# Kernel tuning notes

Hardware: AMD Instinct MI355X
Metric: run time of the kernel (lower is better)

## Reference

```python
import jax, jax.numpy as jnp
import numpy as np

T, D, F, FS, E = 2048, 1024, 2048, 2048, 8
TOP_K = 1


def setup_inputs() -> dict:
    key = jax.random.key(0)
    ks = jax.random.split(key, 8)
    sd = 1.0 / np.sqrt(D)
    sf = 1.0 / np.sqrt(F)
    sfs = 1.0 / np.sqrt(FS)
    return {
        "hidden_states": jax.random.normal(ks[0], (T, D), jnp.float32),
        "router_w": jax.random.normal(ks[1], (E, D), jnp.float32) * sd,     # Linear(D->E), no bias
        "w_gate": jax.random.normal(ks[2], (E, D, F), jnp.float32) * sd,    # fused gate half
        "w_up": jax.random.normal(ks[3], (E, D, F), jnp.float32) * sd,      # fused up half
        "w_down": jax.random.normal(ks[4], (E, F, D), jnp.float32) * sf,
        "ws_gate": jax.random.normal(ks[5], (D, FS), jnp.float32) * sd,
        "ws_up": jax.random.normal(ks[6], (D, FS), jnp.float32) * sd,
        "ws_down": jax.random.normal(ks[7], (FS, D), jnp.float32) * sfs,
    }


def reference(hidden_states, router_w, w_gate, w_up, w_down, ws_gate, ws_up, ws_down):
    # Router: logits -> top-k -> sigmoid of top-k values (Llama4RenormalizeMoeRoutingMethod)
    logits = hidden_states @ router_w.T                      # [T, E]
    top_vals, top_idx = jax.lax.top_k(logits, TOP_K)         # [T, K]
    scores = jax.nn.sigmoid(top_vals.astype(jnp.float32)).astype(hidden_states.dtype)
    # Combine weights [T, E]; apply_router_weight_on_input=True -> scale INPUT per routed copy
    combine = (jax.nn.one_hot(top_idx, E, dtype=hidden_states.dtype) * scores[..., None]).sum(axis=1)
    xe = combine.T[:, :, None] * hidden_states[None]          # [E, T, D] (zero for non-routed tokens)
    g = jnp.einsum('etd,edf->etf', xe, w_gate)
    u = jnp.einsum('etd,edf->etf', xe, w_up)
    routed = jnp.einsum('etf,efd->etd', jax.nn.silu(g) * u, w_down).sum(axis=0)  # [T, D]
    # Shared expert (GatedMLP, SiLU)
    shared = (jax.nn.silu(hidden_states @ ws_gate) * (hidden_states @ ws_up)) @ ws_down
    return shared + routed
```

## Files before the change

### kernel.cpp

```cpp
#include <hip/hip_runtime.h>
#include <hip/hip_bf16.h>
#include <cstdint>
#include <cstddef>

#define T_TOK 2048
#define DIM   1024
#define FDIM  2048
#define NEXP  8

#define GU_MAX 48
#define DN_MAX 64

typedef short  short8  __attribute__((ext_vector_type(8)));
typedef float  floatx4 __attribute__((ext_vector_type(4)));

__device__ inline unsigned short f2bf(float f) {
    unsigned int u = __builtin_bit_cast(unsigned int, f);
    unsigned int r = (u + 0x7FFFu + ((u >> 16) & 1u)) >> 16;
    return (unsigned short)r;
}

__device__ inline unsigned int cvtpk(float a, float b) {
    unsigned int r;
    asm("v_cvt_pk_bf16_f32 %0, %1, %2" : "=v"(r) : "v"(a), "v"(b));
    return r;
}

__device__ inline void glds16(const void* g, const unsigned short* lds_base, int elem_off) {
    int u = __builtin_amdgcn_readfirstlane(elem_off);
    __builtin_amdgcn_global_load_lds(
        (const __attribute__((address_space(1))) unsigned int*)g,
        (__attribute__((address_space(3))) unsigned int*)(lds_base + u), 16, 0, 0);
}

__global__ __launch_bounds__(256) void k_router(
    const float* __restrict__ h, const float* __restrict__ rw,
    int* __restrict__ counts, int* __restrict__ lists,
    unsigned short* __restrict__ hb, unsigned short* __restrict__ xb)
{
    int w = threadIdx.x >> 6, lane = threadIdx.x & 63;
    int t = blockIdx.x * 4 + w;
    const float* hrow = h + (size_t)t * DIM;
    float hv[16];
    #pragma unroll
    for (int i = 0; i < 16; ++i) hv[i] = hrow[lane + 64 * i];
    float acc[NEXP];
    #pragma unroll
    for (int e = 0; e < NEXP; ++e) {
        const float* r = rw + (size_t)e * DIM;
        float s = 0.f;
        #pragma unroll
        for (int i = 0; i < 16; ++i) s += hv[i] * r[lane + 64 * i];
        acc[e] = s;
    }
    #pragma unroll
    for (int e = 0; e < NEXP; ++e) {
        float s = acc[e];
        for (int off = 32; off > 0; off >>= 1) s += __shfl_down(s, off);
        acc[e] = s;
    }
    float score = 0.f;
    if (lane == 0) {
        int be = 0; float bv = acc[0];
        #pragma unroll
        for (int e = 1; e < NEXP; ++e) if (acc[e] > bv) { bv = acc[e]; be = e; }
        score = 1.f / (1.f + __expf(-bv));
        int pos = atomicAdd(&counts[be], 1);
        lists[be * T_TOK + pos] = t;
    }
    score = __shfl(score, 0);
    unsigned short* hbr = hb + (size_t)t * DIM;
    unsigned short* xbr = xb + (size_t)t * DIM;
    #pragma unroll
    for (int i = 0; i < 16; ++i) {
        hbr[lane + 64 * i] = f2bf(hv[i]);
        xbr[lane + 64 * i] = f2bf(score * hv[i]);
    }
}

__global__ void k_schedule(const int* __restrict__ counts,
                           int* __restrict__ gu, int* __restrict__ dn)
{
    if (threadIdx.x != 0 || blockIdx.x != 0) return;
    int n = 0;
    for (int e = 0; e < NEXP; ++e) {
        int c = counts[e];
        for (int r = 0; r < c; r += 128) gu[n++] = (e << 16) | r;
    }
    for (int r = 0; r < T_TOK; r += 128) gu[n++] = (NEXP << 16) | r;
    while (n < GU_MAX) gu[n++] = -1;
    n = 0;
    for (int e = 0; e < NEXP; ++e) {
        int c = counts[e];
        for (int r = 0; r < c; r += 128) {
            dn[n++] = (e << 16) | r;
            dn[n++] = (1 << 28) | (e << 16) | r;
        }
    }
    while (n < DN_MAX) dn[n++] = -1;
}

__global__ __launch_bounds__(256, 2) void k_gateup(
    const unsigned short* __restrict__ xb, const unsigned short* __restrict__ hb,
    const float* __restrict__ w_gate, const float* __restrict__ w_up,
    const float* __restrict__ ws_gate, const float* __restrict__ ws_up,
    const int* __restrict__ counts, const int* __restrict__ lists,
    const int* __restrict__ gu_tiles, unsigned short* __restrict__ Hc)
{
    int ent = gu_tiles[blockIdx.y];
    if (ent < 0) return;
    int e = ent >> 16, row0 = ent & 0xffff;
    bool sh = (e == NEXP);
    int cnt = sh ? T_TOK : counts[e];
    const unsigned short* Asrc = sh ? hb : xb;
    const float* Bg = sh ? ws_gate : w_gate + (size_t)e * DIM * FDIM;
    const float* Bu = sh ? ws_up   : w_up   + (size_t)e * DIM * FDIM;
    int outoff = sh ? FDIM : 0;
    int col0 = blockIdx.x * 128;

    __shared__ int toks[128];
    __shared__ __align__(16) unsigned short As [2][128 * 32];
    __shared__ __align__(16) unsigned short Bgs[2][128 * 40];
    __shared__ __align__(16) unsigned short Bus[2][128 * 40];

    int tid = threadIdx.x;
    if (tid < 128) {
        int r = row0 + tid;
        toks[tid] = (r < cnt) ? (sh ? r : lists[e * T_TOK + r]) : -1;
    }
    __syncthreads();

    int lane = tid & 63, w = tid >> 6;
    int wm = w >> 1, wn = w & 1;

    size_t agoff[2]; int albase[2];
    #pragma unroll
    for (int it = 0; it < 2; ++it) {
        int tt = tid + it * 256;
        int rr = tt >> 2, sq = tt & 3;
        int kg = (sq ^ ((rr >> 1) & 3)) * 8;
        int tk = toks[rr]; if (tk < 0) tk = 0;
        agoff[it] = (size_t)tk * DIM + kg;
        albase[it] = (it * 256 + w * 64) * 8;
    }

    int c = tid & 63;
    int slotW = (w ^ ((c >> 2) & 1)) * 8;
    const float* bgp = Bg + (size_t)(w * 8) * FDIM + col0 + 2 * c;
    const float* bup = Bu + (size_t)(w * 8) * FDIM + col0 + 2 * c;

    float2 gx[8], ux[8];
    auto loadB = [&](int k0) {
        const float* pg = bgp + (size_t)k0 * FDIM;
        const float* pu = bup + (size_t)k0 * FDIM;
        #pragma unroll
        for (int j = 0; j < 8; ++j) {
            gx[j] = *(const float2*)(pg + (size_t)j * FDIM);
            ux[j] = *(const float2*)(pu + (size_t)j * FDIM);
        }
    };
    auto commitB = [&](int p_) {
        unsigned int ge[4], go[4], ue[4], uo[4];
        #pragma unroll
        for (int j = 0; j < 4; ++j) {
            ge[j] = cvtpk(gx[2*j].x, gx[2*j+1].x);
            go[j] = cvtpk(gx[2*j].y, gx[2*j+1].y);
            ue[j] = cvtpk(ux[2*j].x, ux[2*j+1].x);
            uo[j] = cvtpk(ux[2*j].y, ux[2*j+1].y);
        }
        *(uint4*)&Bgs[p_][(2*c)   * 40 + slotW] = make_uint4(ge[0], ge[1], ge[2], ge[3]);
        *(uint4*)&Bgs[p_][(2*c+1) * 40 + slotW] = make_uint4(go[0], go[1], go[2], go[3]);
        *(uint4*)&Bus[p_][(2*c)   * 40 + slotW] = make_uint4(ue[0], ue[1], ue[2], ue[3]);
        *(uint4*)&Bus[p_][(2*c+1) * 40 + slotW] = make_uint4(uo[0], uo[1], uo[2], uo[3]);
    };
    auto loadA = [&](int k0, int p_) {
        #pragma unroll
        for (int it = 0; it < 2; ++it)
            glds16(Asrc + agoff[it] + k0, &As[p_][0], albase[it]);
    };

    floatx4 accg[4][4], accu[4][4];
    #pragma unroll
    for (int mi = 0; mi < 4; ++mi)
    #pragma unroll
    for (int ni = 0; ni < 4; ++ni) {
        floatx4 z = {0.f, 0.f, 0.f, 0.f};
        accg[mi][ni] = z; accu[mi][ni] = z;
    }

    loadA(0, 0);
    loadB(0);
    commitB(0);
    loadB(32);

    int p = 0;
    for (int k0 = 0; k0 < DIM; k0 += 32) {
        asm volatile("s_waitcnt vmcnt(16) lgkmcnt(0)\n\ts_barrier" ::: "memory");
        bool more = (k0 + 32 < DIM);
        if (more) loadA(k0 + 32, p ^ 1);
        __builtin_amdgcn_sched_barrier(0);
        int g = lane >> 4;
        short8 af[4], bgf[4], buf_[4];
        #pragma unroll
        for (int mi = 0; mi < 4; ++mi) {
            int r = wm * 64 + mi * 16 + (lane & 15);
            int slot = (g ^ ((r >> 1) & 3)) * 8;
            af[mi] = *(const short8*)&As[p][r * 32 + slot];
        }
        #pragma unroll
        for (int ni = 0; ni < 4; ++ni) {
            int n = wn * 64 + ni * 16 + (lane & 15);
            int slot = (g ^ ((n >> 3) & 1)) * 8;
            bgf[ni]  = *(const short8*)&Bgs[p][n * 40 + slot];
            buf_[ni] = *(const short8*)&Bus[p][n * 40 + slot];
        }
        if (more) {
            commitB(p ^ 1);
            int nk2 = k0 + 64; if (nk2 >= DIM) nk2 = 0;
            loadB(nk2);
        }
        __builtin_amdgcn_s_setprio(1);
        #pragma unroll
        for (int mi = 0; mi < 4; ++mi)
        #pragma unroll
        for (int ni = 0; ni < 4; ++ni) {
            accg[mi][ni] = __builtin_amdgcn_mfma_f32_16x16x32_bf16(af[mi], bgf[ni],  accg[mi][ni], 0, 0, 0);
            accu[mi][ni] = __builtin_amdgcn_mfma_f32_16x16x32_bf16(af[mi], buf_[ni], accu[mi][ni], 0, 0, 0);
        }
        __builtin_amdgcn_s_setprio(0);
        p ^= 1;
    }

    #pragma unroll
    for (int mi = 0; mi < 4; ++mi)
    #pragma unroll
    for (int ni = 0; ni < 4; ++ni)
    #pragma unroll
    for (int r = 0; r < 4; ++r) {
        int row = wm * 64 + mi * 16 + (lane >> 4) * 4 + r;
        int tok = toks[row];
        if (tok < 0) continue;
        int col = col0 + wn * 64 + ni * 16 + (lane & 15);
        float gv = accg[mi][ni][r], uv = accu[mi][ni][r];
        float hval = (gv / (1.f + __expf(-gv))) * uv;
        Hc[(size_t)tok * (2 * FDIM) + outoff + col] = f2bf(hval);
    }
}

__global__ __launch_bounds__(256, 2) void k_down(
    const unsigned short* __restrict__ Hc,
    const float* __restrict__ w_down, const float* __restrict__ ws_down,
    const int* __restrict__ counts, const int* __restrict__ lists,
    const int* __restrict__ dn_tiles, float* __restrict__ out)
{
    int ent = dn_tiles[blockIdx.y];
    if (ent < 0) return;
    int ks = (ent >> 28) & 1, e = (ent >> 16) & 0xff, row0 = ent & 0xffff;
    int cnt = counts[e];
    const float* B = ks ? ws_down : w_down + (size_t)e * FDIM * DIM;
    int col0 = blockIdx.x * 128;
    size_t abase = (size_t)ks * FDIM;

    __shared__ int toks[128];
    __shared__ __align__(16) unsigned short As[2][128 * 32];
    __shared__ __align__(16) unsigned short Bs[2][128 * 40];

    int tid = threadIdx.x;
    if (tid < 128) {
        int r = row0 + tid;
        toks[tid] = (r < cnt) ? lists[e * T_TOK + r] : -1;
    }
    __syncthreads();

    int lane = tid & 63, w = tid >> 6;
    int wm = w >> 1, wn = w & 1;

    size_t agoff[2]; int albase[2];
    #pragma unroll
    for (int it = 0; it < 2; ++it) {
        int tt = tid + it * 256;
        int rr = tt >> 2, sq = tt & 3;
        int kg = (sq ^ ((rr >> 1) & 3)) * 8;
        int tk = toks[rr]; if (tk < 0) tk = 0;
        agoff[it] = (size_t)tk * (2 * FDIM) + abase + kg;
        albase[it] = (it * 256 + w * 64) * 8;
    }

    int c = tid & 63;
    int slotW = (w ^ ((c >> 2) & 1)) * 8;
    const float* bp_ = B + (size_t)(w * 8) * DIM + col0 + 2 * c;

    float2 bx[8];
    auto loadB = [&](int k0) {
        const float* pb = bp_ + (size_t)k0 * DIM;
        #pragma unroll
        for (int j = 0; j < 8; ++j) bx[j] = *(const float2*)(pb + (size_t)j * DIM);
    };
    auto commitB = [&](int p_) {
        unsigned int be[4], bo[4];
        #pragma unroll
        for (int j = 0; j < 4; ++j) {
            be[j] = cvtpk(bx[2*j].x, bx[2*j+1].x);
            bo[j] = cvtpk(bx[2*j].y, bx[2*j+1].y);
        }
        *(uint4*)&Bs[p_][(2*c)   * 40 + slotW] = make_uint4(be[0], be[1], be[2], be[3]);
        *(uint4*)&Bs[p_][(2*c+1) * 40 + slotW] = make_uint4(bo[0], bo[1], bo[2], bo[3]);
    };
    auto loadA = [&](int k0, int p_) {
        #pragma unroll
        for (int it = 0; it < 2; ++it)
            glds16(Hc + agoff[it] + k0, &As[p_][0], albase[it]);
    };

    floatx4 acc[4][4];
    #pragma unroll
    for (int mi = 0; mi < 4; ++mi)
    #pragma unroll
    for (int ni = 0; ni < 4; ++ni) {
        floatx4 z = {0.f, 0.f, 0.f, 0.f};
        acc[mi][ni] = z;
    }

    loadA(0, 0);
    loadB(0);
    commitB(0);
    loadB(32);

    int p = 0;
    for (int k0 = 0; k0 < FDIM; k0 += 32) {
        asm volatile("s_waitcnt vmcnt(8) lgkmcnt(0)\n\ts_barrier" ::: "memory");
        bool more = (k0 + 32 < FDIM);
        if (more) loadA(k0 + 32, p ^ 1);
        __builtin_amdgcn_sched_barrier(0);
        int g = lane >> 4;
        short8 af[4], bf[4];
        #pragma unroll
        for (int mi = 0; mi < 4; ++mi) {
            int r = wm * 64 + mi * 16 + (lane & 15);
            int slot = (g ^ ((r >> 1) & 3)) * 8;
            af[mi] = *(const short8*)&As[p][r * 32 + slot];
        }
        #pragma unroll
        for (int ni = 0; ni < 4; ++ni) {
            int n = wn * 64 + ni * 16 + (lane & 15);
            int slot = (g ^ ((n >> 3) & 1)) * 8;
            bf[ni] = *(const short8*)&Bs[p][n * 40 + slot];
        }
        if (more) {
            commitB(p ^ 1);
            int nk2 = k0 + 64; if (nk2 >= FDIM) nk2 = 0;
            loadB(nk2);
        }
        __builtin_amdgcn_s_setprio(1);
        #pragma unroll
        for (int mi = 0; mi < 4; ++mi)
        #pragma unroll
        for (int ni = 0; ni < 4; ++ni)
            acc[mi][ni] = __builtin_amdgcn_mfma_f32_16x16x32_bf16(af[mi], bf[ni], acc[mi][ni], 0, 0, 0);
        __builtin_amdgcn_s_setprio(0);
        p ^= 1;
    }

    #pragma unroll
    for (int mi = 0; mi < 4; ++mi)
    #pragma unroll
    for (int ni = 0; ni < 4; ++ni)
    #pragma unroll
    for (int r = 0; r < 4; ++r) {
        int row = wm * 64 + mi * 16 + (lane >> 4) * 4 + r;
        int tok = toks[row];
        if (tok < 0) continue;
        int col = col0 + wn * 64 + ni * 16 + (lane & 15);
        atomicAdd(&out[(size_t)tok * DIM + col], acc[mi][ni][r]);
    }
}

extern "C" void kernel_launch(void* const* d_in, const int* in_sizes, int n_in,
                              void* d_out, int out_size, void* d_ws, size_t ws_size,
                              hipStream_t stream)
{
    const float* h   = (const float*)d_in[0];
    const float* rw  = (const float*)d_in[1];
    const float* wg  = (const float*)d_in[2];
    const float* wu  = (const float*)d_in[3];
    const float* wd  = (const float*)d_in[4];
    const float* wsg = (const float*)d_in[5];
    const float* wsu = (const float*)d_in[6];
    const float* wsd = (const float*)d_in[7];
    float* out = (float*)d_out;

    char* ws = (char*)d_ws;
    int* counts   = (int*)ws;
    int* gu_tiles = (int*)(ws + 256);
    int* dn_tiles = (int*)(ws + 1024);
    int* lists    = (int*)(ws + 2048);
    unsigned short* hb = (unsigned short*)(ws + 131072);
    unsigned short* xb = hb + (size_t)T_TOK * DIM;
    unsigned short* Hc = xb + (size_t)T_TOK * DIM;

    (void)hipMemsetAsync(counts, 0, 64, stream);
    (void)hipMemsetAsync(out, 0, (size_t)T_TOK * DIM * sizeof(float), stream);
    k_router<<<dim3(T_TOK / 4), 256, 0, stream>>>(h, rw, counts, lists, hb, xb);
    k_schedule<<<dim3(1), 64, 0, stream>>>(counts, gu_tiles, dn_tiles);
    k_gateup<<<dim3(FDIM / 128, GU_MAX), 256, 0, stream>>>(
        xb, hb, wg, wu, wsg, wsu, counts, lists, gu_tiles, Hc);
    k_down<<<dim3(DIM / 128, DN_MAX), 256, 0, stream>>>(
        Hc, wd, wsd, counts, lists, dn_tiles, out);
}
```

Baseline: 394.8 us.

## Halve GEMM N-tile to 64 and split down-proj K into four chunks

```diff
diff --git a/kernel.cpp b/kernel.cpp
--- a/kernel.cpp
+++ b/kernel.cpp
@@ -9,7 +9,7 @@
 #define NEXP  8
 
 #define GU_MAX 48
-#define DN_MAX 64
+#define DN_MAX 96
 
 typedef short  short8  __attribute__((ext_vector_type(8)));
 typedef float  floatx4 __attribute__((ext_vector_type(4)));
@@ -92,15 +92,14 @@
     n = 0;
     for (int e = 0; e < NEXP; ++e) {
         int c = counts[e];
-        for (int r = 0; r < c; r += 128) {
-            dn[n++] = (e << 16) | r;
-            dn[n++] = (1 << 28) | (e << 16) | r;
-        }
+        for (int r = 0; r < c; r += 128)
+            for (int kc = 0; kc < 4; ++kc)
+                dn[n++] = (kc << 26) | (e << 16) | r;
     }
     while (n < DN_MAX) dn[n++] = -1;
 }
 
-__global__ __launch_bounds__(256, 2) void k_gateup(
+__global__ __launch_bounds__(256, 4) void k_gateup(
     const unsigned short* __restrict__ xb, const unsigned short* __restrict__ hb,
     const float* __restrict__ w_gate, const float* __restrict__ w_up,
     const float* __restrict__ ws_gate, const float* __restrict__ ws_up,
@@ -116,12 +115,12 @@
     const float* Bg = sh ? ws_gate : w_gate + (size_t)e * DIM * FDIM;
     const float* Bu = sh ? ws_up   : w_up   + (size_t)e * DIM * FDIM;
     int outoff = sh ? FDIM : 0;
-    int col0 = blockIdx.x * 128;
+    int col0 = blockIdx.x * 64;
 
     __shared__ int toks[128];
     __shared__ __align__(16) unsigned short As [2][128 * 32];
-    __shared__ __align__(16) unsigned short Bgs[2][128 * 40];
-    __shared__ __align__(16) unsigned short Bus[2][128 * 40];
+    __shared__ __align__(16) unsigned short Bgs[2][64 * 32];
+    __shared__ __align__(16) unsigned short Bus[2][64 * 32];
 
     int tid = threadIdx.x;
     if (tid < 128) {
@@ -131,7 +130,6 @@
     __syncthreads();
 
     int lane = tid & 63, w = tid >> 6;
-    int wm = w >> 1, wn = w & 1;
 
     size_t agoff[2]; int albase[2];
     #pragma unroll
@@ -145,33 +143,29 @@
     }
 
     int c = tid & 63;
-    int slotW = (w ^ ((c >> 2) & 1)) * 8;
-    const float* bgp = Bg + (size_t)(w * 8) * FDIM + col0 + 2 * c;
-    const float* bup = Bu + (size_t)(w * 8) * FDIM + col0 + 2 * c;
-
-    float2 gx[8], ux[8];
+    int slotW = (w ^ ((c >> 1) & 3)) * 8;
+    const float* bgp = Bg + (size_t)(w * 8) * FDIM + col0 + c;
+    const float* bup = Bu + (size_t)(w * 8) * FDIM + col0 + c;
+
+    float gx[8], ux[8];
     auto loadB = [&](int k0) {
         const float* pg = bgp + (size_t)k0 * FDIM;
         const float* pu = bup + (size_t)k0 * FDIM;
         #pragma unroll
         for (int j = 0; j < 8; ++j) {
-            gx[j] = *(const float2*)(pg + (size_t)j * FDIM);
-            ux[j] = *(const float2*)(pu + (size_t)j * FDIM);
+            gx[j] = pg[(size_t)j * FDIM];
+            ux[j] = pu[(size_t)j * FDIM];
         }
     };
     auto commitB = [&](int p_) {
-        unsigned int ge[4], go[4], ue[4], uo[4];
+        unsigned int gw[4], uw[4];
         #pragma unroll
         for (int j = 0; j < 4; ++j) {
-            ge[j] = cvtpk(gx[2*j].x, gx[2*j+1].x);
-            go[j] = cvtpk(gx[2*j].y, gx[2*j+1].y);
-            ue[j] = cvtpk(ux[2*j].x, ux[2*j+1].x);
-            uo[j] = cvtpk(ux[2*j].y, ux[2*j+1].y);
-        }
-        *(uint4*)&Bgs[p_][(2*c)   * 40 + slotW] = make_uint4(ge[0], ge[1], ge[2], ge[3]);
-        *(uint4*)&Bgs[p_][(2*c+1) * 40 + slotW] = make_uint4(go[0], go[1], go[2], go[3]);
-        *(uint4*)&Bus[p_][(2*c)   * 40 + slotW] = make_uint4(ue[0], ue[1], ue[2], ue[3]);
-        *(uint4*)&Bus[p_][(2*c+1) * 40 + slotW] = make_uint4(uo[0], uo[1], uo[2], uo[3]);
+            gw[j] = cvtpk(gx[2*j], gx[2*j+1]);
+            uw[j] = cvtpk(ux[2*j], ux[2*j+1]);
+        }
+        *(uint4*)&Bgs[p_][c * 32 + slotW] = make_uint4(gw[0], gw[1], gw[2], gw[3]);
+        *(uint4*)&Bus[p_][c * 32 + slotW] = make_uint4(uw[0], uw[1], uw[2], uw[3]);
     };
     auto loadA = [&](int k0, int p_) {
         #pragma unroll
@@ -179,9 +173,9 @@
             glds16(Asrc + agoff[it] + k0, &As[p_][0], albase[it]);
     };
 
-    floatx4 accg[4][4], accu[4][4];
-    #pragma unroll
-    for (int mi = 0; mi < 4; ++mi)
+    floatx4 accg[2][4], accu[2][4];
+    #pragma unroll
+    for (int mi = 0; mi < 2; ++mi)
     #pragma unroll
     for (int ni = 0; ni < 4; ++ni) {
         floatx4 z = {0.f, 0.f, 0.f, 0.f};
@@ -200,19 +194,19 @@
         if (more) loadA(k0 + 32, p ^ 1);
         __builtin_amdgcn_sched_barrier(0);
         int g = lane >> 4;
-        short8 af[4], bgf[4], buf_[4];
-        #pragma unroll
-        for (int mi = 0; mi < 4; ++mi) {
-            int r = wm * 64 + mi * 16 + (lane & 15);
+        short8 af[2], bgf[4], buf_[4];
+        #pragma unroll
+        for (int mi = 0; mi < 2; ++mi) {
+            int r = w * 32 + mi * 16 + (lane & 15);
             int slot = (g ^ ((r >> 1) & 3)) * 8;
             af[mi] = *(const short8*)&As[p][r * 32 + slot];
         }
         #pragma unroll
         for (int ni = 0; ni < 4; ++ni) {
-            int n = wn * 64 + ni * 16 + (lane & 15);
-            int slot = (g ^ ((n >> 3) & 1)) * 8;
-            bgf[ni]  = *(const short8*)&Bgs[p][n * 40 + slot];
-            buf_[ni] = *(const short8*)&Bus[p][n * 40 + slot];
+            int n = ni * 16 + (lane & 15);
+            int slot = (g ^ ((n >> 1) & 3)) * 8;
+            bgf[ni]  = *(const short8*)&Bgs[p][n * 32 + slot];
+            buf_[ni] = *(const short8*)&Bus[p][n * 32 + slot];
         }
         if (more) {
             commitB(p ^ 1);
@@ -221,7 +215,7 @@
         }
         __builtin_amdgcn_s_setprio(1);
         #pragma unroll
-        for (int mi = 0; mi < 4; ++mi)
+        for (int mi = 0; mi < 2; ++mi)
         #pragma unroll
         for (int ni = 0; ni < 4; ++ni) {
             accg[mi][ni] = __builtin_amdgcn_mfma_f32_16x16x32_bf16(af[mi], bgf[ni],  accg[mi][ni], 0, 0, 0);
@@ -232,22 +226,22 @@
     }
 
     #pragma unroll
-    for (int mi = 0; mi < 4; ++mi)
+    for (int mi = 0; mi < 2; ++mi)
     #pragma unroll
     for (int ni = 0; ni < 4; ++ni)
     #pragma unroll
     for (int r = 0; r < 4; ++r) {
-        int row = wm * 64 + mi * 16 + (lane >> 4) * 4 + r;
+        int row = w * 32 + mi * 16 + (lane >> 4) * 4 + r;
         int tok = toks[row];
         if (tok < 0) continue;
-        int col = col0 + wn * 64 + ni * 16 + (lane & 15);
+        int col = col0 + ni * 16 + (lane & 15);
         float gv = accg[mi][ni][r], uv = accu[mi][ni][r];
         float hval = (gv / (1.f + __expf(-gv))) * uv;
         Hc[(size_t)tok * (2 * FDIM) + outoff + col] = f2bf(hval);
     }
 }
 
-__global__ __launch_bounds__(256, 2) void k_down(
+__global__ __launch_bounds__(256, 4) void k_down(
     const unsigned short* __restrict__ Hc,
     const float* __restrict__ w_down, const float* __restrict__ ws_down,
     const int* __restrict__ counts, const int* __restrict__ lists,
@@ -255,15 +249,17 @@
 {
     int ent = dn_tiles[blockIdx.y];
     if (ent < 0) return;
-    int ks = (ent >> 28) & 1, e = (ent >> 16) & 0xff, row0 = ent & 0xffff;
+    int kc = (ent >> 26) & 3, e = (ent >> 16) & 0xff, row0 = ent & 0xffff;
+    int half = kc >> 1, chunk = kc & 1;
     int cnt = counts[e];
-    const float* B = ks ? ws_down : w_down + (size_t)e * FDIM * DIM;
-    int col0 = blockIdx.x * 128;
-    size_t abase = (size_t)ks * FDIM;
+    const float* B = (half ? ws_down : w_down + (size_t)e * FDIM * DIM)
+                     + (size_t)(chunk * 1024) * DIM;
+    int col0 = blockIdx.x * 64;
+    size_t abase = (size_t)(half * FDIM + chunk * 1024);
 
     __shared__ int toks[128];
     __shared__ __align__(16) unsigned short As[2][128 * 32];
-    __shared__ __align__(16) unsigned short Bs[2][128 * 40];
+    __shared__ __align__(16) unsigned short Bs[2][64 * 32];
 
     int tid = threadIdx.x;
     if (tid < 128) {
@@ -273,7 +269,6 @@
     __syncthreads();
 
     int lane = tid & 63, w = tid >> 6;
-    int wm = w >> 1, wn = w & 1;
 
     size_t agoff[2]; int albase[2];
     #pragma unroll
@@ -287,24 +282,20 @@
     }
 
     int c = tid & 63;
-    int slotW = (w ^ ((c >> 2) & 1)) * 8;
-    const float* bp_ = B + (size_t)(w * 8) * DIM + col0 + 2 * c;
-
-    float2 bx[8];
+    int slotW = (w ^ ((c >> 1) & 3)) * 8;
+    const float* bp_ = B + (size_t)(w * 8) * DIM + col0 + c;
+
+    float bx[8];
     auto loadB = [&](int k0) {
         const float* pb = bp_ + (size_t)k0 * DIM;
         #pragma unroll
-        for (int j = 0; j < 8; ++j) bx[j] = *(const float2*)(pb + (size_t)j * DIM);
+        for (int j = 0; j < 8; ++j) bx[j] = pb[(size_t)j * DIM];
     };
     auto commitB = [&](int p_) {
-        unsigned int be[4], bo[4];
-        #pragma unroll
-        for (int j = 0; j < 4; ++j) {
-            be[j] = cvtpk(bx[2*j].x, bx[2*j+1].x);
-            bo[j] = cvtpk(bx[2*j].y, bx[2*j+1].y);
-        }
-        *(uint4*)&Bs[p_][(2*c)   * 40 + slotW] = make_uint4(be[0], be[1], be[2], be[3]);
-        *(uint4*)&Bs[p_][(2*c+1) * 40 + slotW] = make_uint4(bo[0], bo[1], bo[2], bo[3]);
+        unsigned int bw[4];
+        #pragma unroll
+        for (int j = 0; j < 4; ++j) bw[j] = cvtpk(bx[2*j], bx[2*j+1]);
+        *(uint4*)&Bs[p_][c * 32 + slotW] = make_uint4(bw[0], bw[1], bw[2], bw[3]);
     };
     auto loadA = [&](int k0, int p_) {
         #pragma unroll
@@ -312,9 +303,9 @@
             glds16(Hc + agoff[it] + k0, &As[p_][0], albase[it]);
     };
 
-    floatx4 acc[4][4];
-    #pragma unroll
-    for (int mi = 0; mi < 4; ++mi)
+    floatx4 acc[2][4];
+    #pragma unroll
+    for (int mi = 0; mi < 2; ++mi)
     #pragma unroll
     for (int ni = 0; ni < 4; ++ni) {
         floatx4 z = {0.f, 0.f, 0.f, 0.f};
@@ -327,33 +318,33 @@
     loadB(32);
 
     int p = 0;
-    for (int k0 = 0; k0 < FDIM; k0 += 32) {
+    for (int k0 = 0; k0 < 1024; k0 += 32) {
         asm volatile("s_waitcnt vmcnt(8) lgkmcnt(0)\n\ts_barrier" ::: "memory");
-        bool more = (k0 + 32 < FDIM);
+        bool more = (k0 + 32 < 1024);
         if (more) loadA(k0 + 32, p ^ 1);
         __builtin_amdgcn_sched_barrier(0);
         int g = lane >> 4;
-        short8 af[4], bf[4];
-        #pragma unroll
-        for (int mi = 0; mi < 4; ++mi) {
-            int r = wm * 64 + mi * 16 + (lane & 15);
+        short8 af[2], bf[4];
+        #pragma unroll
+        for (int mi = 0; mi < 2; ++mi) {
+            int r = w * 32 + mi * 16 + (lane & 15);
             int slot = (g ^ ((r >> 1) & 3)) * 8;
             af[mi] = *(const short8*)&As[p][r * 32 + slot];
         }
         #pragma unroll
         for (int ni = 0; ni < 4; ++ni) {
-            int n = wn * 64 + ni * 16 + (lane & 15);
-            int slot = (g ^ ((n >> 3) & 1)) * 8;
-            bf[ni] = *(const short8*)&Bs[p][n * 40 + slot];
+            int n = ni * 16 + (lane & 15);
+            int slot = (g ^ ((n >> 1) & 3)) * 8;
+            bf[ni] = *(const short8*)&Bs[p][n * 32 + slot];
         }
         if (more) {
             commitB(p ^ 1);
-            int nk2 = k0 + 64; if (nk2 >= FDIM) nk2 = 0;
+            int nk2 = k0 + 64; if (nk2 >= 1024) nk2 = 0;
             loadB(nk2);
         }
         __builtin_amdgcn_s_setprio(1);
         #pragma unroll
-        for (int mi = 0; mi < 4; ++mi)
+        for (int mi = 0; mi < 2; ++mi)
         #pragma unroll
         for (int ni = 0; ni < 4; ++ni)
             acc[mi][ni] = __builtin_amdgcn_mfma_f32_16x16x32_bf16(af[mi], bf[ni], acc[mi][ni], 0, 0, 0);
@@ -362,15 +353,15 @@
     }
 
     #pragma unroll
-    for (int mi = 0; mi < 4; ++mi)
+    for (int mi = 0; mi < 2; ++mi)
     #pragma unroll
     for (int ni = 0; ni < 4; ++ni)
     #pragma unroll
     for (int r = 0; r < 4; ++r) {
-        int row = wm * 64 + mi * 16 + (lane >> 4) * 4 + r;
+        int row = w * 32 + mi * 16 + (lane >> 4) * 4 + r;
         int tok = toks[row];
         if (tok < 0) continue;
-        int col = col0 + wn * 64 + ni * 16 + (lane & 15);
+        int col = col0 + ni * 16 + (lane & 15);
         atomicAdd(&out[(size_t)tok * DIM + col], acc[mi][ni][r]);
     }
 }
@@ -402,8 +393,8 @@
     (void)hipMemsetAsync(out, 0, (size_t)T_TOK * DIM * sizeof(float), stream);
     k_router<<<dim3(T_TOK / 4), 256, 0, stream>>>(h, rw, counts, lists, hb, xb);
     k_schedule<<<dim3(1), 64, 0, stream>>>(counts, gu_tiles, dn_tiles);
-    k_gateup<<<dim3(FDIM / 128, GU_MAX), 256, 0, stream>>>(
+    k_gateup<<<dim3(FDIM / 64, GU_MAX), 256, 0, stream>>>(
         xb, hb, wg, wu, wsg, wsu, counts, lists, gu_tiles, Hc);
-    k_down<<<dim3(DIM / 128, DN_MAX), 256, 0, stream>>>(
+    k_down<<<dim3(DIM / 64, DN_MAX), 256, 0, stream>>>(
         Hc, wd, wsd, counts, lists, dn_tiles, out);
 }
```

After: 547.3 us. 38.6% more time.
